# Optimization experiments

Hardware: AMD Instinct MI355X
Metric: run time of the kernel (lower is better)

## Reference

```python
import jax, jax.numpy as jnp
import numpy as np

HIDDEN = 256
MAX_POS = 2000  # table has MAX_POS + 1 rows


def get_sinusoid_encoding_table(n_position, d_hid):
    pos = np.arange(n_position, dtype=np.float64)[:, None]
    i = np.arange(d_hid)[None, :]
    angle = pos / np.power(10000.0, 2.0 * (i // 2) / d_hid)
    table = np.zeros((n_position, d_hid), dtype=np.float32)
    table[:, 0::2] = np.sin(angle[:, 0::2])
    table[:, 1::2] = np.cos(angle[:, 1::2])
    return jnp.asarray(table)


def setup_inputs() -> dict:
    key = jax.random.key(0)
    k1, k2 = jax.random.split(key)
    B, T = 64, 160
    x = jax.random.normal(k1, (B, T, HIDDEN), dtype=jnp.float32)
    duration = jax.random.randint(k2, (B, T), 0, 12, dtype=jnp.int64 if jax.config.jax_enable_x64 else jnp.int32)
    position_enc = get_sinusoid_encoding_table(MAX_POS + 1, HIDDEN)
    return {"x": x, "position_enc": position_enc, "duration": duration, "max_len": 2000}


def reference(x, position_enc, duration, max_len):
    # x: [B, T, H], duration: [B, T] ints, max_len: python int
    B, T, H = x.shape
    csum = jnp.cumsum(duration, axis=1)            # inclusive cumsum [B, T]
    excl = csum - duration                          # exclusive cumsum [B, T]
    mel_len = csum[:, -1]                           # [B]
    frames = jnp.arange(max_len)                    # [L]
    # token index owning each output frame: smallest t with csum[t] > frame
    idx = jax.vmap(lambda c: jnp.searchsorted(c, frames, side='right'))(csum)  # [B, L]
    idx = jnp.minimum(idx, T - 1)
    valid = frames[None, :] < mel_len[:, None]      # [B, L]
    # gather expanded features
    out = jnp.take_along_axis(x, idx[..., None], axis=1)          # [B, L, H]
    # per-token local position -> sinusoid table row
    pos_within = frames[None, :] - jnp.take_along_axis(excl, idx, axis=1)  # [B, L]
    pos_within = jnp.where(valid, pos_within, 0)
    pos = position_enc[pos_within]                                 # [B, L, H]
    out = jnp.where(valid[..., None], out, 0.0)
    pos = jnp.where(valid[..., None], pos, 0.0)
    return out, pos, mel_len
```

## Files before the change

### kernel.cpp

```cpp
#include <hip/hip_runtime.h>

constexpr int B      = 64;
constexpr int T      = 160;
constexpr int H      = 256;
constexpr int MAXLEN = 2000;
constexpr int FPB    = 16;
constexpr int NTH    = 256;

typedef float floatx4 __attribute__((ext_vector_type(4)));

__global__ __launch_bounds__(NTH) void build_map_kernel(
    const int* __restrict__ duration,
    int*       __restrict__ map,
    float*     __restrict__ out)
{
    __shared__ int s_scan[NTH];
    const int b   = blockIdx.x;
    const int tid = threadIdx.x;

    int d = (tid < T) ? duration[b * T + tid] : 0;
    s_scan[tid] = d;
    __syncthreads();
    #pragma unroll
    for (int off = 1; off < NTH; off <<= 1) {
        int v   = s_scan[tid];
        int add = (tid >= off) ? s_scan[tid - off] : 0;
        __syncthreads();
        s_scan[tid] = v + add;
        __syncthreads();
    }
    const int csum    = s_scan[tid];
    const int excl    = csum - d;
    const int mel_len = s_scan[T - 1];

    if (tid == 0)
        out[(size_t)2 * B * MAXLEN * H + b] = (float)mel_len;

    int* bm = map + b * MAXLEN;

    for (int f = mel_len + tid; f < MAXLEN; f += NTH)
        bm[f] = -1;

    if (tid < T) {
        for (int f = excl; f < csum; ++f)
            bm[f] = (tid << 8) | (f - excl);
    }
}

__global__ __launch_bounds__(NTH) void expand_kernel(
    const float* __restrict__ x,
    const float* __restrict__ pos_enc,
    const int*   __restrict__ map,
    float*       __restrict__ out)
{
    const int tid  = threadIdx.x;
    const int b    = blockIdx.y;
    const int wave = tid >> 6;
    const int lane = tid & 63;

    const size_t out_base = (size_t)b * MAXLEN * H;
    const size_t pos_base = (size_t)B * MAXLEN * H + out_base;
    const int f0 = blockIdx.x * FPB;
    const int* bm = map + b * MAXLEN;

    #pragma unroll
    for (int i = 0; i < FPB / 4; ++i) {
        const int f = f0 + wave + 4 * i;
        const int m = bm[f];

        floatx4 xo = (floatx4)0.f;
        floatx4 po = (floatx4)0.f;
        if (m >= 0) {
            const int t  = m >> 8;
            const int pw = m & 255;
            xo = ((const floatx4*)(x       + ((size_t)b * T + t) * H))[lane];
            po = ((const floatx4*)(pos_enc + (size_t)pw      * H))[lane];
        }
        __builtin_nontemporal_store(xo, (floatx4*)(out + out_base + (size_t)f * H) + lane);
        __builtin_nontemporal_store(po, (floatx4*)(out + pos_base + (size_t)f * H) + lane);
    }
}

__global__ __launch_bounds__(NTH) void lr_kernel(
    const float* __restrict__ x,
    const float* __restrict__ pos_enc,
    const int*   __restrict__ duration,
    float*       __restrict__ out)
{
    __shared__ int s_scan[NTH];
    __shared__ int s_csum[T];
    __shared__ int s_excl[T];

    const int b   = blockIdx.y;
    const int tid = threadIdx.x;

    int d = (tid < T) ? duration[b * T + tid] : 0;
    s_scan[tid] = d;
    __syncthreads();
    #pragma unroll
    for (int off = 1; off < NTH; off <<= 1) {
        int v   = s_scan[tid];
        int add = (tid >= off) ? s_scan[tid - off] : 0;
        __syncthreads();
        s_scan[tid] = v + add;
        __syncthreads();
    }
    if (tid < T) {
        s_csum[tid] = s_scan[tid];
        s_excl[tid] = s_scan[tid] - d;
    }
    __syncthreads();

    const int mel_len = s_csum[T - 1];
    if (blockIdx.x == 0 && tid == 0) {
        out[(size_t)2 * B * MAXLEN * H + b] = (float)mel_len;
    }

    const int wave = tid >> 6;
    const int lane = tid & 63;
    const size_t out_base = (size_t)b * MAXLEN * H;
    const size_t pos_base = (size_t)B * MAXLEN * H + out_base;
    const int f0 = blockIdx.x * FPB;

    for (int i = wave; i < FPB; i += 4) {
        const int f = f0 + i;
        if (f >= MAXLEN) break;
        const bool valid = (f < mel_len);

        int lo = 0, hi = T;
        while (lo < hi) {
            int mid = (lo + hi) >> 1;
            if (s_csum[mid] <= f) lo = mid + 1; else hi = mid;
        }
        const int idx = min(lo, T - 1);

        float4 xo = make_float4(0.f, 0.f, 0.f, 0.f);
        float4 po = xo;
        if (valid) {
            const int pw = f - s_excl[idx];
            xo = ((const float4*)(x + ((size_t)b * T + idx) * H))[lane];
            po = ((const float4*)(pos_enc + (size_t)pw * H))[lane];
        }
        ((float4*)(out + out_base + (size_t)f * H))[lane] = xo;
        ((float4*)(out + pos_base + (size_t)f * H))[lane] = po;
    }
}

extern "C" void kernel_launch(void* const* d_in, const int* in_sizes, int n_in,
                              void* d_out, int out_size, void* d_ws, size_t ws_size,
                              hipStream_t stream)
{
    const float* x        = (const float*)d_in[0];
    const float* pos_enc  = (const float*)d_in[1];
    const int*   duration = (const int*)d_in[2];
    float*       out      = (float*)d_out;

    const size_t map_bytes = (size_t)B * MAXLEN * sizeof(int);
    if (d_ws != nullptr && ws_size >= map_bytes) {
        int* map = (int*)d_ws;
        build_map_kernel<<<dim3(B), NTH, 0, stream>>>(duration, map, out);
        expand_kernel<<<dim3(MAXLEN / FPB, B), NTH, 0, stream>>>(x, pos_enc, map, out);
    } else {
        dim3 grid((MAXLEN + FPB - 1) / FPB, B);
        lr_kernel<<<grid, NTH, 0, stream>>>(x, pos_enc, duration, out);
    }
}
```

Measured before the change: 279.6 us.

## Batch expand loads per wave, use persistent grid-stride tiles and regular stores

Each wave now reads four consecutive map entries with a single int4 load. It issues all four x and pos_enc row loads unconditionally, clamping invalid entries to row 0, then writes results masked by multiplying with 0 or 1. This is meant to raise memory-level parallelism and remove branch divergence. The grid shrinks to 32 blocks per batch, with each block looping over tiles grid-stride style, and nontemporal stores are replaced by ordinary stores. The cost is wasted loads for padded frames, fewer blocks in flight, and possible cache pollution from the output writes.

```diff
diff --git a/kernel.cpp b/kernel.cpp
--- a/kernel.cpp
+++ b/kernel.cpp
@@ -6,8 +6,7 @@
 constexpr int MAXLEN = 2000;
 constexpr int FPB    = 16;
 constexpr int NTH    = 256;
-
-typedef float floatx4 __attribute__((ext_vector_type(4)));
+constexpr int TPB_X  = 32;
 
 __global__ __launch_bounds__(NTH) void build_map_kernel(
     const int* __restrict__ duration,
@@ -58,26 +57,35 @@
     const int wave = tid >> 6;
     const int lane = tid & 63;
 
-    const size_t out_base = (size_t)b * MAXLEN * H;
-    const size_t pos_base = (size_t)B * MAXLEN * H + out_base;
-    const int f0 = blockIdx.x * FPB;
-    const int* bm = map + b * MAXLEN;
+    const float* xb   = x   + (size_t)b * T * H;
+    float*       outb = out + (size_t)b * MAXLEN * H;
+    float*       posb = outb + (size_t)B * MAXLEN * H;
+    const int*   bm   = map + b * MAXLEN;
 
-    #pragma unroll
-    for (int i = 0; i < FPB / 4; ++i) {
-        const int f = f0 + wave + 4 * i;
-        const int m = bm[f];
+    constexpr int NTILE = MAXLEN / FPB;
+    for (int tx = blockIdx.x; tx < NTILE; tx += TPB_X) {
+        const int fw = tx * FPB + 4 * wave;
+        const int4 m4 = *(const int4*)(bm + fw);
+        const int mm[4] = { m4.x, m4.y, m4.z, m4.w };
 
-        floatx4 xo = (floatx4)0.f;
-        floatx4 po = (floatx4)0.f;
-        if (m >= 0) {
-            const int t  = m >> 8;
-            const int pw = m & 255;
-            xo = ((const floatx4*)(x       + ((size_t)b * T + t) * H))[lane];
-            po = ((const floatx4*)(pos_enc + (size_t)pw      * H))[lane];
+        float4 xo[4], po[4];
+        #pragma unroll
+        for (int j = 0; j < 4; ++j) {
+            const int msel = (mm[j] < 0) ? 0 : mm[j];
+            const int t  = msel >> 8;
+            const int pw = msel & 255;
+            xo[j] = ((const float4*)(xb      + (size_t)t  * H))[lane];
+            po[j] = ((const float4*)(pos_enc + (size_t)pw * H))[lane];
         }
-        __builtin_nontemporal_store(xo, (floatx4*)(out + out_base + (size_t)f * H) + lane);
-        __builtin_nontemporal_store(po, (floatx4*)(out + pos_base + (size_t)f * H) + lane);
+        #pragma unroll
+        for (int j = 0; j < 4; ++j) {
+            const float s = (mm[j] >= 0) ? 1.0f : 0.0f;
+            const int   f = fw + j;
+            float4 a = make_float4(xo[j].x * s, xo[j].y * s, xo[j].z * s, xo[j].w * s);
+            float4 p = make_float4(po[j].x * s, po[j].y * s, po[j].z * s, po[j].w * s);
+            ((float4*)(outb + (size_t)f * H))[lane] = a;
+            ((float4*)(posb + (size_t)f * H))[lane] = p;
+        }
     }
 }
 
@@ -159,7 +167,7 @@
     if (d_ws != nullptr && ws_size >= map_bytes) {
         int* map = (int*)d_ws;
         build_map_kernel<<<dim3(B), NTH, 0, stream>>>(duration, map, out);
-        expand_kernel<<<dim3(MAXLEN / FPB, B), NTH, 0, stream>>>(x, pos_enc, map, out);
+        expand_kernel<<<dim3(TPB_X, B), NTH, 0, stream>>>(x, pos_enc, map, out);
     } else {
         dim3 grid((MAXLEN + FPB - 1) / FPB, B);
         lr_kernel<<<grid, NTH, 0, stream>>>(x, pos_enc, duration, out);
```

New measurement: 272.6 us. 1.03x faster.
